# Performance work log

Hardware: AMD Instinct MI355X
Metric: run time of the kernel (lower is better)

The kernel has to match this reference:

```python
import jax, jax.numpy as jnp
import numpy as np

BS, MA, H, NH = 64, 64, 64, 4  # molecules, max atoms per molecule, hsize, n_heads


def _lengths():
    # deterministic ragged molecule sizes in [24, 64]
    return np.array([24 + (7 * i) % 41 for i in range(BS)], dtype=np.int64)


def _scopes():
    lengths = _lengths()
    N = int(lengths.sum())  # 2774
    scope = np.zeros((BS, MA), dtype=np.int64)      # pad slots gather row 0 (zeros)
    rev = np.zeros((N,), dtype=np.int64)            # flat atom -> b*MA + slot
    pos = 1                                          # flat row 0 is the zero pad row
    for b, L in enumerate(lengths):
        scope[b, :L] = np.arange(pos, pos + L)
        rev[pos - 1:pos - 1 + L] = b * MA + np.arange(L)
        pos += L
    return scope, rev, N


def setup_inputs() -> dict:
    key = jax.random.key(0)
    k0, k1, k2, k3 = jax.random.split(key, 4)
    scope, rev, N = _scopes()
    inputs = jax.random.normal(k0, (N + 1, H), dtype=jnp.float32)
    inputs = inputs.at[0].set(0.0)  # zero pad row, as in graphretro flat tensors
    Wa_pair = jax.random.normal(k1, (H, H * NH), dtype=jnp.float32) * (1.0 / np.sqrt(H))
    Wa_score = jax.random.normal(k2, (H, NH), dtype=jnp.float32) * (1.0 / np.sqrt(H))
    W_proj = jax.random.normal(k3, (H * NH, H), dtype=jnp.float32) * (1.0 / np.sqrt(H * NH))
    return {
        "inputs": inputs,
        "scope_tensor": jnp.asarray(scope),
        "scope_rev_tensor": jnp.asarray(rev),
        "Wa_pair": Wa_pair,
        "Wa_score": Wa_score,
        "W_proj": W_proj,
    }


def reference(inputs, scope_tensor, scope_rev_tensor, Wa_pair, Wa_score, W_proj):
    bs, ma = scope_tensor.shape
    h = inputs.shape[1]
    nh = Wa_score.shape[1]
    # flat_to_batch: [bs, ma, h]; pad slots pull the zero row 0
    c_batch = inputs[scope_tensor]
    # get_pair: pairwise sum of atom embeddings -> [bs, ma, ma, h]
    atom_pair = c_batch[:, :, None, :] + c_batch[:, None, :, :]
    # Wa_pair (no bias) + relu, viewed as [bs, ma, ma, h, nh]
    total_att = jax.nn.relu(atom_pair @ Wa_pair).reshape(bs, ma, ma, h, nh)
    # einsum '...hn,hjn->...jn' with j==1, then sigmoid -> [bs, ma, ma, nh]
    att_score = jax.nn.sigmoid(jnp.einsum('bijhn,hn->bijn', total_att, Wa_score))
    # att_score * c_atom[b,j,h], summed over j -> [bs, ma, h, nh]
    c_sum = jnp.einsum('bijn,bjh->bihn', att_score, c_batch)
    # view to [bs, ma, h*nh] (h-major, matching torch .view) and project
    c_atom_att = c_sum.reshape(bs, ma, h * nh) @ W_proj  # [bs, ma, h]
    c_mol_att = c_atom_att.sum(axis=1)  # [bs, h]
    # batch_to_flat + prepend zero row -> [N+1, h]
    flat = c_atom_att.reshape(bs * ma, h)[scope_rev_tensor]
    c_atom_att_flat = jnp.concatenate([jnp.zeros((1, h), flat.dtype), flat], axis=0)
    return (c_mol_att, c_atom_att_flat)
```

## Files before the change

kernel.cpp:

```cpp
#include <hip/hip_runtime.h>
#include <stdint.h>

typedef _Float16 h2 __attribute__((ext_vector_type(2)));
typedef _Float16 h8 __attribute__((ext_vector_type(8)));
typedef float f32x4 __attribute__((ext_vector_type(4)));
typedef unsigned int u32;
typedef unsigned short u16;

#define CB_STR  72
#define WA_STR  68
#define WP_STR  68
#define P_STR   68
#define CW_STR  68
#define ABF_STR 264

__device__ __forceinline__ u32 pk2(float a, float b) {
    return __builtin_bit_cast(u32, __builtin_amdgcn_cvt_pkrtz(a, b));
}
__device__ __forceinline__ h8 frag4(u32 a, u32 b, u32 c, u32 d) {
    return __builtin_bit_cast(h8, make_uint4(a, b, c, d));
}

union SMemU {
    struct { u16 wa[4][64 * WA_STR]; u16 wp[4][64 * WP_STR]; } p1;
    u16 ab[64 * ABF_STR];
};

__global__ __launch_bounds__(512, 1) void atom_attn(
    const float* __restrict__ inputs,
    const int*   __restrict__ scope,
    const float* __restrict__ Wa_pair,
    const float* __restrict__ Wa_score,
    const float* __restrict__ W_proj,
    float* __restrict__ out_mol,
    float* __restrict__ out_flat)
{
    __shared__ __align__(16) SMemU s_u;
    __shared__ __align__(16) u16 s_cb[64 * CB_STR];
    __shared__ __align__(16) u16 s_p [4][64 * P_STR];
    __shared__ __align__(16) u16 s_cw[4][64 * CW_STR];
    __shared__ __align__(16) u32 s_ws[4 * 32];
    __shared__ __align__(16) float s_msum[8][16];

    const int t = threadIdx.x;
    const int w = t >> 6, l = t & 63;
    const int ml = l & 15, q = l >> 4;
    const int b = blockIdx.x;

    {
        const int hp = t >> 4;
        const int cc = (t & 15) * 16;
        const float* r0p = Wa_pair + (2 * hp) * 256 + cc;
        const float* r1p = Wa_pair + (2 * hp + 1) * 256 + cc;
        #pragma unroll
        for (int v = 0; v < 4; ++v) {
            const f32x4 x0 = *(const f32x4*)(r0p + v * 4);
            const f32x4 x1 = *(const f32x4*)(r1p + v * 4);
            #pragma unroll
            for (int e = 0; e < 4; ++e) {
                const int c = cc + v * 4 + e;
                const int n = c & 3, ho = c >> 2;
                *(u32*)&s_u.p1.wa[n][ho * WA_STR + 2 * hp] = pk2(x0[e], x1[e]);
            }
        }
    }
    {
        const int n = t >> 7, r = t & 127;
        const int hh = r >> 2, o0 = (r & 3) * 16;
        const float* c0p = W_proj + (8 * hh + n) * 64 + o0;
        const float* c1p = W_proj + (8 * hh + 4 + n) * 64 + o0;
        #pragma unroll
        for (int v = 0; v < 4; ++v) {
            const f32x4 x0 = *(const f32x4*)(c0p + v * 4);
            const f32x4 x1 = *(const f32x4*)(c1p + v * 4);
            #pragma unroll
            for (int e = 0; e < 4; ++e) {
                const int o = o0 + v * 4 + e;
                *(u32*)&s_u.p1.wp[n][o * WP_STR + 2 * hh] = pk2(x0[e], x1[e]);
            }
        }
    }
    if (t < 256) {
        const int jp = (t & 31) * 2;
        const int pp = t >> 5;
        const int r0 = scope[b * 64 + jp];
        const int r1 = scope[b * 64 + jp + 1];
        const f32x4 a0 = *(const f32x4*)(inputs + (size_t)r0 * 64 + pp * 8);
        const f32x4 a1 = *(const f32x4*)(inputs + (size_t)r0 * 64 + pp * 8 + 4);
        const f32x4 b0 = *(const f32x4*)(inputs + (size_t)r1 * 64 + pp * 8);
        const f32x4 b1 = *(const f32x4*)(inputs + (size_t)r1 * 64 + pp * 8 + 4);
        *(uint4*)&s_cb[jp * CB_STR + pp * 8] =
            make_uint4(pk2(a0[0], a0[1]), pk2(a0[2], a0[3]), pk2(a1[0], a1[1]), pk2(a1[2], a1[3]));
        *(uint4*)&s_cb[(jp + 1) * CB_STR + pp * 8] =
            make_uint4(pk2(b0[0], b0[1]), pk2(b0[2], b0[3]), pk2(b1[0], b1[1]), pk2(b1[2], b1[3]));
    }
    if (t < 128) {
        const int n = t >> 5, hh = t & 31;
        s_ws[n * 32 + hh] = pk2(Wa_score[(2 * hh) * 4 + n], Wa_score[(2 * hh + 1) * 4 + n]);
    }
    if (b == 0 && t < 64) out_flat[t] = 0.f;
    __syncthreads();

    if (w < 4) {
        const int n = w;
        f32x4 D[4][4];
        #pragma unroll
        for (int mt = 0; mt < 4; ++mt)
            #pragma unroll
            for (int jt = 0; jt < 4; ++jt) D[mt][jt] = (f32x4)0.f;
        #pragma unroll
        for (int ks = 0; ks < 2; ++ks) {
            h8 bfj[4];
            #pragma unroll
            for (int jt = 0; jt < 4; ++jt)
                bfj[jt] = __builtin_bit_cast(h8,
                    *(const uint4*)&s_cb[(jt * 16 + ml) * CB_STR + ks * 32 + q * 8]);
            #pragma unroll
            for (int mt = 0; mt < 4; ++mt) {
                const uint2 x0 = *(const uint2*)&s_u.p1.wa[n][(mt * 16 + ml) * WA_STR + ks * 32 + q * 8];
                const uint2 x1 = *(const uint2*)&s_u.p1.wa[n][(mt * 16 + ml) * WA_STR + ks * 32 + q * 8 + 4];
                const h8 af = frag4(x0.x, x0.y, x1.x, x1.y);
                #pragma unroll
                for (int jt = 0; jt < 4; ++jt)
                    D[mt][jt] = __builtin_amdgcn_mfma_f32_16x16x32_f16(af, bfj[jt], D[mt][jt], 0, 0, 0);
            }
        }
        #pragma unroll
        for (int mt = 0; mt < 4; ++mt)
            #pragma unroll
            for (int jt = 0; jt < 4; ++jt) {
                const int j = jt * 16 + ml;
                *(uint2*)&s_p[n][j * P_STR + mt * 16 + q * 4] =
                    make_uint2(pk2(D[mt][jt][0], D[mt][jt][1]), pk2(D[mt][jt][2], D[mt][jt][3]));
            }
    } else {
        const int n = w - 4;
        f32x4 D[4][4];
        #pragma unroll
        for (int mt = 0; mt < 4; ++mt)
            #pragma unroll
            for (int ot = 0; ot < 4; ++ot) D[mt][ot] = (f32x4)0.f;
        #pragma unroll
        for (int ks = 0; ks < 2; ++ks) {
            h8 afm[4];
            #pragma unroll
            for (int mt = 0; mt < 4; ++mt)
                afm[mt] = __builtin_bit_cast(h8,
                    *(const uint4*)&s_cb[(mt * 16 + ml) * CB_STR + ks * 32 + q * 8]);
            #pragma unroll
            for (int ot = 0; ot < 4; ++ot) {
                const uint2 y0 = *(const uint2*)&s_u.p1.wp[n][(ot * 16 + ml) * WP_STR + ks * 32 + q * 8];
                const uint2 y1 = *(const uint2*)&s_u.p1.wp[n][(ot * 16 + ml) * WP_STR + ks * 32 + q * 8 + 4];
                const h8 bf = frag4(y0.x, y0.y, y1.x, y1.y);
                #pragma unroll
                for (int mt = 0; mt < 4; ++mt)
                    D[mt][ot] = __builtin_amdgcn_mfma_f32_16x16x32_f16(afm[mt], bf, D[mt][ot], 0, 0, 0);
            }
        }
        #pragma unroll
        for (int mt = 0; mt < 4; ++mt)
            #pragma unroll
            for (int ot = 0; ot < 4; ++ot) {
                const int o = ot * 16 + ml;
                *(uint2*)&s_cw[n][o * CW_STR + mt * 16 + q * 4] =
                    make_uint2(pk2(D[mt][ot][0], D[mt][ot][1]), pk2(D[mt][ot][2], D[mt][ot][3]));
            }
    }
    __syncthreads();

    {
        const int n = w & 3, ih = w >> 2;
        u32 pj_u[32];
        #pragma unroll
        for (int k = 0; k < 16; ++k) {
            const uint2 vv = *(const uint2*)&s_p[n][l * P_STR + k * 4];
            pj_u[2 * k] = vv.x; pj_u[2 * k + 1] = vv.y;
        }
        u32 ws_u[32];
        #pragma unroll
        for (int k = 0; k < 8; ++k) {
            const uint4 vv = *(const uint4*)&s_ws[n * 32 + k * 4];
            ws_u[4 * k] = vv.x; ws_u[4 * k + 1] = vv.y;
            ws_u[4 * k + 2] = vv.z; ws_u[4 * k + 3] = vv.w;
        }
        const h2 zero2 = {(_Float16)0.f, (_Float16)0.f};
        #pragma unroll 4
        for (int ii = 0; ii < 32; ++ii) {
            const int i = ih * 32 + ii;
            const u16* pir = &s_p[n][i * P_STR];
            float s0 = 0.f, s1 = 0.f;
            #pragma unroll
            for (int c8 = 0; c8 < 8; ++c8) {
                const uint2 u0 = *(const uint2*)&pir[c8 * 8];
                const uint2 u1 = *(const uint2*)&pir[c8 * 8 + 4];
                const u32 pe[4] = {u0.x, u0.y, u1.x, u1.y};
                #pragma unroll
                for (int e = 0; e < 4; ++e) {
                    const h2 pi2 = __builtin_bit_cast(h2, pe[e]);
                    const h2 pj2 = __builtin_bit_cast(h2, pj_u[c8 * 4 + e]);
                    h2 tv = pi2 + pj2;
                    tv = __builtin_elementwise_max(tv, zero2);
                    if (e & 1)
                        s1 = __builtin_amdgcn_fdot2(tv,
                                __builtin_bit_cast(h2, ws_u[c8 * 4 + e]), s1, false);
                    else
                        s0 = __builtin_amdgcn_fdot2(tv,
                                __builtin_bit_cast(h2, ws_u[c8 * 4 + e]), s0, false);
                }
            }
            const float s = s0 + s1;
            const float a = 1.f / (1.f + __expf(-s));
            const _Float16 ah = (_Float16)a;
            s_u.ab[i * ABF_STR + n * 64 + l] = __builtin_bit_cast(u16, ah);
        }
    }
    __syncthreads();

    {
        const int nt = w >> 1, mh = w & 1;
        f32x4 D3[2];
        D3[0] = (f32x4)0.f; D3[1] = (f32x4)0.f;
        #pragma unroll
        for (int ks = 0; ks < 8; ++ks) {
            const int n = ks >> 1;
            const uint2 y0 = *(const uint2*)&s_cw[n][(nt * 16 + ml) * CW_STR + (ks & 1) * 32 + q * 8];
            const uint2 y1 = *(const uint2*)&s_cw[n][(nt * 16 + ml) * CW_STR + (ks & 1) * 32 + q * 8 + 4];
            const h8 bf = frag4(y0.x, y0.y, y1.x, y1.y);
            #pragma unroll
            for (int mtl = 0; mtl < 2; ++mtl) {
                const int mt = mh * 2 + mtl;
                const h8 af = __builtin_bit_cast(h8,
                    *(const uint4*)&s_u.ab[(mt * 16 + ml) * ABF_STR + ks * 32 + q * 8]);
                D3[mtl] = __builtin_amdgcn_mfma_f32_16x16x32_f16(af, bf, D3[mtl], 0, 0, 0);
            }
        }
        const int o = nt * 16 + ml;
        float colsum = 0.f;
        #pragma unroll
        for (int mtl = 0; mtl < 2; ++mtl)
            #pragma unroll
            for (int r = 0; r < 4; ++r) {
                const int i = (mh * 2 + mtl) * 16 + q * 4 + r;
                const int row = scope[b * 64 + i];
                if (row > 0) out_flat[(size_t)row * 64 + o] = D3[mtl][r];
                colsum += D3[mtl][r];
            }
        colsum += __shfl_xor(colsum, 16, 64);
        colsum += __shfl_xor(colsum, 32, 64);
        if (l < 16) s_msum[w][ml] = colsum;
    }
    __syncthreads();
    if (t < 64)
        out_mol[b * 64 + t] = s_msum[2 * (t >> 4)][t & 15] + s_msum[2 * (t >> 4) + 1][t & 15];
}

extern "C" void kernel_launch(void* const* d_in, const int* in_sizes, int n_in,
                              void* d_out, int out_size, void* d_ws, size_t ws_size,
                              hipStream_t stream) {
    const float* inputs   = (const float*)d_in[0];
    const int*   scope    = (const int*)d_in[1];
    const float* Wa_pair  = (const float*)d_in[3];
    const float* Wa_score = (const float*)d_in[4];
    const float* W_proj   = (const float*)d_in[5];
    float* out = (float*)d_out;

    dim3 grid(64);
    atom_attn<<<grid, 512, 0, stream>>>(inputs, scope, Wa_pair, Wa_score,
                                        W_proj, out, out + 64 * 64);
}
```

Before: 84.89 us.

## Split each molecule across four blocks by query-row quarter with atomic mol sums

Launches a 4x64 grid so each block handles 16 of the 64 query rows of one molecule, cutting the per-block attention-score loop from 32 to 8 rows per wave and using more CUs than the earlier 64 blocks. The molecule sum is accumulated with atomicAdd into an output zeroed by a memset before launch, which also covers the zero pad row. Each block still redoes the full per-molecule setup (weight staging, pair GEMM, c*W GEMM), so that work is now done four times, and the extra memset adds a launch.

```diff
diff --git a/kernel.cpp b/kernel.cpp
--- a/kernel.cpp
+++ b/kernel.cpp
@@ -23,7 +23,7 @@
 
 union SMemU {
     struct { u16 wa[4][64 * WA_STR]; u16 wp[4][64 * WP_STR]; } p1;
-    u16 ab[64 * ABF_STR];
+    u16 ab[16 * ABF_STR];
 };
 
 __global__ __launch_bounds__(512, 1) void atom_attn(
@@ -40,12 +40,12 @@
     __shared__ __align__(16) u16 s_p [4][64 * P_STR];
     __shared__ __align__(16) u16 s_cw[4][64 * CW_STR];
     __shared__ __align__(16) u32 s_ws[4 * 32];
-    __shared__ __align__(16) float s_msum[8][16];
 
     const int t = threadIdx.x;
     const int w = t >> 6, l = t & 63;
     const int ml = l & 15, q = l >> 4;
-    const int b = blockIdx.x;
+    const int bx = blockIdx.x;
+    const int b  = blockIdx.y;
 
     {
         const int hp = t >> 4;
@@ -98,7 +98,6 @@
         const int n = t >> 5, hh = t & 31;
         s_ws[n * 32 + hh] = pk2(Wa_score[(2 * hh) * 4 + n], Wa_score[(2 * hh + 1) * 4 + n]);
     }
-    if (b == 0 && t < 64) out_flat[t] = 0.f;
     __syncthreads();
 
     if (w < 4) {
@@ -184,9 +183,10 @@
             ws_u[4 * k + 2] = vv.z; ws_u[4 * k + 3] = vv.w;
         }
         const h2 zero2 = {(_Float16)0.f, (_Float16)0.f};
-        #pragma unroll 4
-        for (int ii = 0; ii < 32; ++ii) {
-            const int i = ih * 32 + ii;
+        #pragma unroll
+        for (int ii = 0; ii < 8; ++ii) {
+            const int i_loc = ih * 8 + ii;
+            const int i = bx * 16 + i_loc;
             const u16* pir = &s_p[n][i * P_STR];
             float s0 = 0.f, s1 = 0.f;
             #pragma unroll
@@ -211,47 +211,36 @@
             const float s = s0 + s1;
             const float a = 1.f / (1.f + __expf(-s));
             const _Float16 ah = (_Float16)a;
-            s_u.ab[i * ABF_STR + n * 64 + l] = __builtin_bit_cast(u16, ah);
+            s_u.ab[i_loc * ABF_STR + n * 64 + l] = __builtin_bit_cast(u16, ah);
         }
     }
     __syncthreads();
 
-    {
-        const int nt = w >> 1, mh = w & 1;
-        f32x4 D3[2];
-        D3[0] = (f32x4)0.f; D3[1] = (f32x4)0.f;
+    if (w < 4) {
+        f32x4 D = (f32x4)0.f;
         #pragma unroll
         for (int ks = 0; ks < 8; ++ks) {
             const int n = ks >> 1;
-            const uint2 y0 = *(const uint2*)&s_cw[n][(nt * 16 + ml) * CW_STR + (ks & 1) * 32 + q * 8];
-            const uint2 y1 = *(const uint2*)&s_cw[n][(nt * 16 + ml) * CW_STR + (ks & 1) * 32 + q * 8 + 4];
+            const h8 af = __builtin_bit_cast(h8,
+                *(const uint4*)&s_u.ab[ml * ABF_STR + ks * 32 + q * 8]);
+            const uint2 y0 = *(const uint2*)&s_cw[n][(w * 16 + ml) * CW_STR + (ks & 1) * 32 + q * 8];
+            const uint2 y1 = *(const uint2*)&s_cw[n][(w * 16 + ml) * CW_STR + (ks & 1) * 32 + q * 8 + 4];
             const h8 bf = frag4(y0.x, y0.y, y1.x, y1.y);
-            #pragma unroll
-            for (int mtl = 0; mtl < 2; ++mtl) {
-                const int mt = mh * 2 + mtl;
-                const h8 af = __builtin_bit_cast(h8,
-                    *(const uint4*)&s_u.ab[(mt * 16 + ml) * ABF_STR + ks * 32 + q * 8]);
-                D3[mtl] = __builtin_amdgcn_mfma_f32_16x16x32_f16(af, bf, D3[mtl], 0, 0, 0);
-            }
-        }
-        const int o = nt * 16 + ml;
+            D = __builtin_amdgcn_mfma_f32_16x16x32_f16(af, bf, D, 0, 0, 0);
+        }
+        const int o = w * 16 + ml;
         float colsum = 0.f;
         #pragma unroll
-        for (int mtl = 0; mtl < 2; ++mtl)
-            #pragma unroll
-            for (int r = 0; r < 4; ++r) {
-                const int i = (mh * 2 + mtl) * 16 + q * 4 + r;
-                const int row = scope[b * 64 + i];
-                if (row > 0) out_flat[(size_t)row * 64 + o] = D3[mtl][r];
-                colsum += D3[mtl][r];
-            }
+        for (int r = 0; r < 4; ++r) {
+            const int i_loc = q * 4 + r;
+            const int row = scope[b * 64 + bx * 16 + i_loc];
+            if (row > 0) out_flat[(size_t)row * 64 + o] = D[r];
+            colsum += D[r];
+        }
         colsum += __shfl_xor(colsum, 16, 64);
         colsum += __shfl_xor(colsum, 32, 64);
-        if (l < 16) s_msum[w][ml] = colsum;
-    }
-    __syncthreads();
-    if (t < 64)
-        out_mol[b * 64 + t] = s_msum[2 * (t >> 4)][t & 15] + s_msum[2 * (t >> 4) + 1][t & 15];
+        if (l < 16) atomicAdd(out_mol + b * 64 + o, colsum);
+    }
 }
 
 extern "C" void kernel_launch(void* const* d_in, const int* in_sizes, int n_in,
@@ -264,7 +253,9 @@
     const float* W_proj   = (const float*)d_in[5];
     float* out = (float*)d_out;
 
-    dim3 grid(64);
+    (void)hipMemsetAsync(d_out, 0, (64 * 64 + 64) * sizeof(float), stream);
+
+    dim3 grid(4, 64);
     atom_attn<<<grid, 512, 0, stream>>>(inputs, scope, Wa_pair, Wa_score,
                                         W_proj, out, out + 64 * 64);
 }
```

New measurement: 74.03 us. 1.15x faster.
